# Kernel tuning notes

Measured on AMD Instinct MI355X. Metric: run time of the kernel, lower is better.

The kernel has to match this reference:

```python
import jax, jax.numpy as jnp
import numpy as np

# Ragged layout: 8 sequences packed into total_tokens=6144 tokens.
_SEQLENS = [1024, 512, 1024, 256, 768, 1024, 512, 1024]
_TOTAL = sum(_SEQLENS)  # 6144
_H, _D = 16, 128
_MAXLEN = 1024


def setup_inputs() -> dict:
    key = jax.random.key(0)
    kq, kk, kv = jax.random.split(key, 3)
    cu = jnp.asarray(np.concatenate([[0], np.cumsum(_SEQLENS)]), dtype=jnp.int32)
    return {
        "q": jax.random.normal(kq, (_TOTAL, _H, _D), dtype=jnp.float32),
        "k": jax.random.normal(kk, (_TOTAL, _H, _D), dtype=jnp.float32),
        "v": jax.random.normal(kv, (_TOTAL, _H, _D), dtype=jnp.float32),
        "cu_seqlens_q": cu,
        "cu_seqlens_k": cu,
        "max_seqlen_q": _MAXLEN,
        "max_seqlen_k": _MAXLEN,
    }


def _pad_gather(x, cu, L):
    """Gather packed [T,h,d] into padded [B,L,h,d] plus validity mask [B,L]."""
    starts = cu[:-1]                                   # [B]
    lens = cu[1:] - cu[:-1]                            # [B]
    pos = jnp.arange(L, dtype=cu.dtype)                # [L]
    idx = starts[:, None] + pos[None, :]               # [B,L]
    mask = pos[None, :] < lens[:, None]                # [B,L]
    idx = jnp.clip(idx, 0, x.shape[0] - 1)
    return x[idx], mask, jnp.where(mask, idx, x.shape[0])


def reference(q, k, v, cu_seqlens_q, cu_seqlens_k, max_seqlen_q, max_seqlen_k):
    # Equivalent to pytorch_varlen_attention: per-sequence SDPA (non-causal,
    # no dropout), vectorized via pad-to-max + key masking.
    T, h, d = q.shape
    qp, mq, idx_q = _pad_gather(q, cu_seqlens_q, max_seqlen_q)  # [B,Lq,h,d]
    kp, mk, _ = _pad_gather(k, cu_seqlens_k, max_seqlen_k)      # [B,Lk,h,d]
    vp, _, _ = _pad_gather(v, cu_seqlens_k, max_seqlen_k)

    scale = 1.0 / jnp.sqrt(jnp.asarray(d, dtype=q.dtype))
    scores = jnp.einsum("bqhd,bkhd->bhqk", qp, kp) * scale      # [B,h,Lq,Lk]
    neg = jnp.asarray(jnp.finfo(scores.dtype).min, scores.dtype)
    scores = jnp.where(mk[:, None, None, :], scores, neg)
    attn = jax.nn.softmax(scores, axis=-1)
    out_pad = jnp.einsum("bhqk,bkhd->bqhd", attn, vp)           # [B,Lq,h,d]

    # Scatter valid rows back to packed layout; invalid rows dropped (idx==T).
    out = jnp.zeros((T, h, d), dtype=q.dtype)
    out = out.at[idx_q.reshape(-1)].set(
        out_pad.reshape(-1, h, d), mode="drop")
    return out
```

## Files before the change

### kernel.cpp

```cpp
#include <hip/hip_runtime.h>
#include <hip/hip_bf16.h>
#include <stdint.h>

#define H 16
#define D 128
#define BM 256
#define BN 64
#define NW 8
#define NT 512

typedef __bf16 bf16_t;
typedef bf16_t bf16x8 __attribute__((ext_vector_type(8)));
typedef bf16_t bf16x2 __attribute__((ext_vector_type(2)));
typedef float f32x16 __attribute__((ext_vector_type(16)));

#define MFMA32(a, b, c) __builtin_amdgcn_mfma_f32_32x32x16_bf16(a, b, c, 0, 0, 0)

union FragU { uint32_t w[4]; bf16x8 v; };

static __device__ __forceinline__ uint32_t cvtpk_bf16(float lo, float hi) {
  uint32_t r;
  asm("v_cvt_pk_bf16_f32 %0, %1, %2" : "=v"(r) : "v"(lo), "v"(hi));
  return r;
}

static __device__ __forceinline__ void gld_lds16(const bf16_t* g, bf16_t* l) {
  __builtin_amdgcn_global_load_lds(
      (const __attribute__((address_space(1))) void*)g,
      (__attribute__((address_space(3))) void*)l, 16, 0, 0);
}


__global__ void conv_k(const float* __restrict__ kin, bf16_t* __restrict__ kb, int n8) {
  int i = blockIdx.x * blockDim.x + threadIdx.x;
  int stride = gridDim.x * blockDim.x;
  for (; i < n8; i += stride) {
    const float* p = kin + (size_t)i * 8;
    float4 a = *(const float4*)p, b = *(const float4*)(p + 4);
    bf16x8 w;
    w[0] = (bf16_t)a.x; w[1] = (bf16_t)a.y; w[2] = (bf16_t)a.z; w[3] = (bf16_t)a.w;
    w[4] = (bf16_t)b.x; w[5] = (bf16_t)b.y; w[6] = (bf16_t)b.z; w[7] = (bf16_t)b.w;
    *(bf16x8*)(kb + (size_t)i * 8) = w;
  }
}

__global__ void conv_vt(const float* __restrict__ v, bf16_t* __restrict__ vt,
                        const int* __restrict__ cuk, int nseq) {
  int tile = blockIdx.x, h = blockIdx.y;
  int acc = 0, seq = -1, lt = 0, s0k = 0, Lk = 0, Lkp = 0;
  size_t vb = 0;
  for (int s = 0; s < nseq; ++s) {
    int Ls = cuk[s + 1] - cuk[s];
    int Lp = (Ls + 63) & ~63;
    int nt = Lp / 64;
    if (tile < acc + nt) { seq = s; lt = tile - acc; s0k = cuk[s]; Lk = Ls; Lkp = Lp; break; }
    acc += nt; vb += (size_t)H * D * Lp;
  }
  if (seq < 0) return;
  int kv0 = lt * 64;
  int d = threadIdx.x;
  bf16x8 w[8];
  #pragma unroll
  for (int j = 0; j < 64; ++j) {
    int kv = kv0 + j;
    int kvc = kv < Lk ? kv : Lk - 1;
    float val = v[((size_t)(s0k + kvc) * H + h) * D + d];
    w[j >> 3][j & 7] = (bf16_t)val;
  }
  bf16_t* dstT = vt + vb + (size_t)h * D * Lkp + (size_t)lt * 8192;
  #pragma unroll
  for (int c = 0; c < 8; ++c)
    *(bf16x8*)(dstT + ((size_t)c * 128 + d) * 8) = w[c];
}


__global__ __launch_bounds__(NT, 2)
void fa_varlen11(const float* __restrict__ q,
                 const bf16_t* __restrict__ kb,
                 const bf16_t* __restrict__ vt,
                 const int* __restrict__ cuq,
                 const int* __restrict__ cuk,
                 float* __restrict__ out,
                 int nseq, int maxtiles)
{
  __shared__ alignas(16) bf16_t sK[3][BN * D];
  __shared__ alignas(16) bf16_t sVt[2][8 * 128 * 8];

  const int nwg = gridDim.x;
  const int orig = blockIdx.x;
  const int qq = nwg >> 3, rr = nwg & 7;
  const int xcd = orig & 7;
  const int wgid = (xcd < rr ? xcd * (qq + 1) : rr * (qq + 1) + (xcd - rr) * qq) + (orig >> 3);
  const int tile = wgid % maxtiles;
  const int h = wgid / maxtiles;

  int acc = 0, seq = -1, lt = 0, s0q = 0, s0k = 0, Lq = 0, Lk = 0, Lkp = 0;
  size_t vb = 0;
  for (int s = 0; s < nseq; ++s) {
    int a = cuq[s], b = cuq[s + 1];
    int Ls = b - a;
    int nt = (Ls + BM - 1) / BM;
    int Lks = cuk[s + 1] - cuk[s];
    int Lp = (Lks + 63) & ~63;
    if (tile < acc + nt) {
      seq = s; lt = tile - acc; s0q = a; Lq = Ls;
      s0k = cuk[s]; Lk = Lks; Lkp = Lp;
      break;
    }
    acc += nt; vb += (size_t)H * D * Lp;
  }
  if (seq < 0) return;

  const int q0 = lt * BM;
  const int tid = threadIdx.x;
  const int lane = tid & 63;
  const int lq = lane & 31;
  const int hi = lane >> 5;

  const float SC = 0.08838834764831845f * 1.44269504088896340f;

  bf16x8 qf[8];
  {
    int warp = tid >> 6;
    int qrow = q0 + warp * 32 + lq; if (qrow >= Lq) qrow = Lq - 1;
    const float* qp = q + ((size_t)(s0q + qrow) * H + h) * D;
    #pragma unroll
    for (int ks = 0; ks < 8; ++ks) {
      const float* p = qp + ks * 16 + hi * 8;
      float4 a = *(const float4*)p, b = *(const float4*)(p + 4);
      bf16x8 r;
      r[0] = (bf16_t)(a.x * SC); r[1] = (bf16_t)(a.y * SC);
      r[2] = (bf16_t)(a.z * SC); r[3] = (bf16_t)(a.w * SC);
      r[4] = (bf16_t)(b.x * SC); r[5] = (bf16_t)(b.y * SC);
      r[6] = (bf16_t)(b.z * SC); r[7] = (bf16_t)(b.w * SC);
      qf[ks] = r;
    }
  }

  const bf16_t* vsrcH = vt + vb + (size_t)h * D * Lkp;

  auto STAGE_K = [&](int tt, int buf) {
    const int kvb = tt * BN;
    #pragma unroll
    for (int i = 0; i < 2; ++i) {
      int g = tid + i * NT;
      int row = g >> 4, cc = g & 15;
      int kvr = kvb + row; if (kvr >= Lk) kvr = Lk - 1;
      const bf16_t* src = kb + ((size_t)(s0k + kvr) * H + h) * D + ((cc ^ (row & 7)) << 3);
      gld_lds16(src, &sK[buf][g * 8]);
    }
  };
  auto STAGE_V = [&](int tt, int buf) {
    const bf16_t* vsrc = vsrcH + (size_t)tt * 8192;
    #pragma unroll
    for (int i = 0; i < 2; ++i) {
      int g = tid + i * NT;
      gld_lds16(vsrc + (size_t)g * 8, &sVt[buf][g * 8]);
    }
  };

  f32x16 oacc[4];
  #pragma unroll
  for (int dt = 0; dt < 4; ++dt)
    #pragma unroll
    for (int r = 0; r < 16; ++r) oacc[dt][r] = 0.f;
  float m = -1e30f, l = 0.f;

  const int nkv = (Lk + BN - 1) / BN;

  STAGE_K(0, 0);
  STAGE_V(0, 0);
  STAGE_K(nkv > 1 ? 1 : 0, 1);
  asm volatile("s_waitcnt vmcnt(2)" ::: "memory");
  __builtin_amdgcn_s_barrier();
  __builtin_amdgcn_sched_barrier(0);

  for (int t = 0; t < nkv; ++t) {
    const int kvb = t * BN;
    int tV = t + 1 < nkv ? t + 1 : nkv - 1;
    int tK = t + 2 < nkv ? t + 2 : nkv - 1;
    STAGE_V(tV, (t + 1) & 1);
    STAGE_K(tK, (t + 2) % 3);

    const bf16_t* sKc = sK[t % 3];
    const bf16_t* sVc = sVt[t & 1];
    const bool tail = (kvb + BN > Lk);

    #pragma unroll
    for (int ct = 0; ct < 2; ++ct) {
      f32x16 sa, sb;
      #pragma unroll
      for (int r = 0; r < 16; ++r) { sa[r] = 0.f; sb[r] = 0.f; }
      int krow = ct * 32 + lq;
      __builtin_amdgcn_s_setprio(1);
      #pragma unroll
      for (int ks = 0; ks < 4; ++ks) {
        int posa = (ks * 2 + hi) ^ (krow & 7);
        bf16x8 kfa = *(const bf16x8*)&sKc[krow * 128 + (posa << 3)];
        sa = MFMA32(kfa, qf[ks], sa);
        int posb = ((ks + 4) * 2 + hi) ^ (krow & 7);
        bf16x8 kfb = *(const bf16x8*)&sKc[krow * 128 + (posb << 3)];
        sb = MFMA32(kfb, qf[ks + 4], sb);
      }
      __builtin_amdgcn_s_setprio(0);

      f32x16 st;
      #pragma unroll
      for (int r = 0; r < 16; ++r) {
        float x = sa[r] + sb[r];
        if (tail) {
          int kvi = kvb + ct * 32 + (r & 3) + 8 * (r >> 2) + 4 * hi;
          if (kvi >= Lk) x = -1e30f;
        }
        st[r] = x;
      }
      float m0;
      {
        float a0 = fmaxf(st[0], st[1]),  a1 = fmaxf(st[2], st[3]);
        float a2 = fmaxf(st[4], st[5]),  a3 = fmaxf(st[6], st[7]);
        float a4 = fmaxf(st[8], st[9]),  a5 = fmaxf(st[10], st[11]);
        float a6 = fmaxf(st[12], st[13]), a7 = fmaxf(st[14], st[15]);
        float b0 = fmaxf(a0, a1), b1 = fmaxf(a2, a3);
        float b2 = fmaxf(a4, a5), b3 = fmaxf(a6, a7);
        m0 = fmaxf(fmaxf(b0, b1), fmaxf(b2, b3));
      }
      float m1 = fmaxf(m0, __shfl_xor(m0, 32));
      bool trig = m1 > m + 8.0f;
      float mnew = trig ? m1 : m;
      float alpha = __builtin_amdgcn_exp2f(m - mnew);
      m = mnew;

      #pragma unroll
      for (int r = 0; r < 16; ++r)
        st[r] = __builtin_amdgcn_exp2f(st[r] - m);
      float psum;
      {
        float a0 = st[0] + st[1],  a1 = st[2] + st[3];
        float a2 = st[4] + st[5],  a3 = st[6] + st[7];
        float a4 = st[8] + st[9],  a5 = st[10] + st[11];
        float a6 = st[12] + st[13], a7 = st[14] + st[15];
        float b0 = a0 + a1, b1 = a2 + a3, b2 = a4 + a5, b3 = a6 + a7;
        psum = (b0 + b1) + (b2 + b3);
      }
      psum += __shfl_xor(psum, 32);
      l = l * alpha + psum;

      if (__any(alpha != 1.0f)) {
        #pragma unroll
        for (int r = 0; r < 16; ++r) {
          int cr = (r & 3) + 8 * (r >> 2) + 4 * hi;
          float a2 = __shfl(alpha, cr);
          #pragma unroll
          for (int dt = 0; dt < 4; ++dt) oacc[dt][r] *= a2;
        }
      }

      uint32_t c0 = cvtpk_bf16(st[0],  st[1]),  c1 = cvtpk_bf16(st[2],  st[3]);
      uint32_t c2 = cvtpk_bf16(st[4],  st[5]),  c3 = cvtpk_bf16(st[6],  st[7]);
      uint32_t c4 = cvtpk_bf16(st[8],  st[9]),  c5 = cvtpk_bf16(st[10], st[11]);
      uint32_t c6 = cvtpk_bf16(st[12], st[13]), c7 = cvtpk_bf16(st[14], st[15]);
      { auto rr2 = __builtin_amdgcn_permlane32_swap(c0, c2, false, false); c0 = rr2[0]; c2 = rr2[1]; }
      { auto rr2 = __builtin_amdgcn_permlane32_swap(c1, c3, false, false); c1 = rr2[0]; c3 = rr2[1]; }
      { auto rr2 = __builtin_amdgcn_permlane32_swap(c4, c6, false, false); c4 = rr2[0]; c6 = rr2[1]; }
      { auto rr2 = __builtin_amdgcn_permlane32_swap(c5, c7, false, false); c5 = rr2[0]; c7 = rr2[1]; }
      FragU pa, pb;
      pa.w[0] = c0; pa.w[1] = c1; pa.w[2] = c2; pa.w[3] = c3;
      pb.w[0] = c4; pb.w[1] = c5; pb.w[2] = c6; pb.w[3] = c7;

      __builtin_amdgcn_s_setprio(1);
      #pragma unroll
      for (int dt = 0; dt < 4; ++dt) {
        int drow = dt * 32 + lq;
        bf16x8 vf0 = *(const bf16x8*)&sVc[((ct * 4 + hi) * 128 + drow) << 3];
        oacc[dt] = MFMA32(pa.v, vf0, oacc[dt]);
        bf16x8 vf1 = *(const bf16x8*)&sVc[((ct * 4 + 2 + hi) * 128 + drow) << 3];
        oacc[dt] = MFMA32(pb.v, vf1, oacc[dt]);
      }
      __builtin_amdgcn_s_setprio(0);
    }

    asm volatile("s_waitcnt vmcnt(2)" ::: "memory");
    __builtin_amdgcn_s_barrier();
    __builtin_amdgcn_sched_barrier(0);
  }

  #pragma unroll
  for (int r = 0; r < 16; ++r) {
    int cr = (r & 3) + 8 * (r >> 2) + 4 * hi;
    int warp = tid >> 6;
    int qr = q0 + warp * 32 + cr;
    float lcr = __shfl(l, cr);
    if (qr < Lq) {
      float rn = 1.0f / lcr;
      float* op = out + ((size_t)(s0q + qr) * H + h) * D + lq;
      #pragma unroll
      for (int dt = 0; dt < 4; ++dt)
        op[dt * 32] = oacc[dt][r] * rn;
    }
  }
}


__global__ __launch_bounds__(256, 3)
void fa_varlen2(const float* __restrict__ q,
                const float* __restrict__ k,
                const float* __restrict__ v,
                const int* __restrict__ cuq,
                const int* __restrict__ cuk,
                float* __restrict__ out,
                int nseq)
{
  __shared__ alignas(16) bf16_t sBuf[128 * 128];
  __shared__ float sRed[4 * 32];
  bf16_t* sK  = sBuf;
  bf16_t* sVt = sBuf + 64 * 128;

  const int tile = blockIdx.x;
  const int h = blockIdx.y;

  int acc = 0, seq = -1, lt = 0, s0q = 0, s0k = 0, Lq = 0, Lk = 0;
  for (int s = 0; s < nseq; ++s) {
    int a = cuq[s], b = cuq[s + 1];
    int Ls = b - a;
    int nt = (Ls + 127) / 128;
    if (tile < acc + nt) {
      seq = s; lt = tile - acc; s0q = a; Lq = Ls;
      s0k = cuk[s]; Lk = cuk[s + 1] - s0k;
      break;
    }
    acc += nt;
  }
  if (seq < 0) return;

  const int q0 = lt * 128;
  const int tid = threadIdx.x;
  const int warp = tid >> 6;
  const int lane = tid & 63;
  const int lq = lane & 31;
  const int hi = lane >> 5;

  const float SC = 0.08838834764831845f * 1.44269504088896340f;

  #pragma unroll
  for (int ii = 0; ii < 8; ++ii) {
    int g = tid + ii * 256;
    int row = g >> 4, cc = g & 15;
    int gr = q0 + row; if (gr >= Lq) gr = Lq - 1;
    const float* p = q + ((size_t)(s0q + gr) * H + h) * D + cc * 8;
    float4 f0 = *(const float4*)p;
    float4 f1 = *(const float4*)(p + 4);
    bf16x8 w;
    w[0] = (bf16_t)f0.x; w[1] = (bf16_t)f0.y; w[2] = (bf16_t)f0.z; w[3] = (bf16_t)f0.w;
    w[4] = (bf16_t)f1.x; w[5] = (bf16_t)f1.y; w[6] = (bf16_t)f1.z; w[7] = (bf16_t)f1.w;
    *(bf16x8*)&sBuf[row * 128 + (((cc ^ (row & 7))) << 3)] = w;
  }
  __syncthreads();

  bf16x8 qf[8];
  {
    int row = warp * 32 + lq;
    #pragma unroll
    for (int ks = 0; ks < 8; ++ks) {
      int pos = (ks * 2 + hi) ^ (row & 7);
      qf[ks] = *(const bf16x8*)&sBuf[row * 128 + (pos << 3)];
    }
  }

  f32x16 oacc[4];
  #pragma unroll
  for (int dt = 0; dt < 4; ++dt)
    #pragma unroll
    for (int r = 0; r < 16; ++r) oacc[dt][r] = 0.f;
  float m = -1e30f, l = 0.f;

  const int nkv = (Lk + 63) / 64;
  for (int it = 0; it < nkv; ++it) {
    const int kv0 = it * 64;
    __syncthreads();

    #pragma unroll
    for (int ii = 0; ii < 4; ++ii) {
      int g = tid + ii * 256;
      int row = g >> 4, cc = g & 15;
      int gr = kv0 + row; if (gr >= Lk) gr = Lk - 1;
      const float* p = k + ((size_t)(s0k + gr) * H + h) * D + cc * 8;
      float4 f0 = *(const float4*)p;
      float4 f1 = *(const float4*)(p + 4);
      bf16x8 w;
      w[0] = (bf16_t)f0.x; w[1] = (bf16_t)f0.y; w[2] = (bf16_t)f0.z; w[3] = (bf16_t)f0.w;
      w[4] = (bf16_t)f1.x; w[5] = (bf16_t)f1.y; w[6] = (bf16_t)f1.z; w[7] = (bf16_t)f1.w;
      *(bf16x8*)&sK[row * 128 + (((cc ^ (row & 7))) << 3)] = w;
    }
    {
      int kp = tid & 31;
      int seg = tid >> 5;
      int r0 = kv0 + 2 * kp, r1 = r0 + 1;
      if (r0 >= Lk) r0 = Lk - 1;
      if (r1 >= Lk) r1 = Lk - 1;
      const float* p0 = v + ((size_t)(s0k + r0) * H + h) * D + seg * 16;
      const float* p1 = v + ((size_t)(s0k + r1) * H + h) * D + seg * 16;
      float va[16], vbf[16];
      *(float4*)&va[0]  = *(const float4*)p0;
      *(float4*)&va[4]  = *(const float4*)(p0 + 4);
      *(float4*)&va[8]  = *(const float4*)(p0 + 8);
      *(float4*)&va[12] = *(const float4*)(p0 + 12);
      *(float4*)&vbf[0]  = *(const float4*)p1;
      *(float4*)&vbf[4]  = *(const float4*)(p1 + 4);
      *(float4*)&vbf[8]  = *(const float4*)(p1 + 8);
      *(float4*)&vbf[12] = *(const float4*)(p1 + 12);
      int kvr = 2 * kp;
      #pragma unroll
      for (int i = 0; i < 16; ++i) {
        int d = seg * 16 + i;
        int pos = (kp >> 2) ^ (d & 7);
        bf16x2 w2; w2[0] = (bf16_t)va[i]; w2[1] = (bf16_t)vbf[i];
        *(bf16x2*)&sVt[d * 64 + (pos << 3) + (kvr & 7)] = w2;
      }
    }
    __syncthreads();

    const bool tail = (kv0 + 64 > Lk);

    #pragma unroll
    for (int ct = 0; ct < 2; ++ct) {
      f32x16 st;
      #pragma unroll
      for (int r = 0; r < 16; ++r) st[r] = 0.f;
      int krow = ct * 32 + lq;
      #pragma unroll
      for (int ks = 0; ks < 8; ++ks) {
        int pos = (ks * 2 + hi) ^ (krow & 7);
        bf16x8 kf = *(const bf16x8*)&sK[krow * 128 + (pos << 3)];
        st = MFMA32(kf, qf[ks], st);
      }

      float tmax = -1e30f;
      #pragma unroll
      for (int r = 0; r < 16; ++r) {
        float x = st[r] * SC;
        if (tail) {
          int kvi = kv0 + ct * 32 + (r & 3) + 8 * (r >> 2) + 4 * hi;
          if (kvi >= Lk) x = -1e30f;
        }
        st[r] = x;
        tmax = fmaxf(tmax, x);
      }
      tmax = fmaxf(tmax, __shfl_xor(tmax, 32));
      bool trig = tmax > m + 8.0f;
      float mnew = trig ? tmax : m;
      float alpha = exp2f(m - mnew);
      m = mnew;

      float psum = 0.f;
      #pragma unroll
      for (int r = 0; r < 16; ++r) {
        float e = exp2f(st[r] - m);
        st[r] = e;
        psum += e;
      }
      psum += __shfl_xor(psum, 32);
      l = l * alpha + psum;

      if (__any(alpha != 1.0f)) {
        if (hi == 0) sRed[warp * 32 + lq] = alpha;
        asm volatile("s_waitcnt lgkmcnt(0)" ::: "memory");
        #pragma unroll
        for (int r = 0; r < 16; ++r) {
          float a2 = sRed[warp * 32 + (r & 3) + 8 * (r >> 2) + 4 * hi];
          #pragma unroll
          for (int dt = 0; dt < 4; ++dt) oacc[dt][r] *= a2;
        }
      }

      uint32_t c0 = cvtpk_bf16(st[0],  st[1]),  c1 = cvtpk_bf16(st[2],  st[3]);
      uint32_t c2 = cvtpk_bf16(st[4],  st[5]),  c3 = cvtpk_bf16(st[6],  st[7]);
      uint32_t c4 = cvtpk_bf16(st[8],  st[9]),  c5 = cvtpk_bf16(st[10], st[11]);
      uint32_t c6 = cvtpk_bf16(st[12], st[13]), c7 = cvtpk_bf16(st[14], st[15]);
      { auto rr2 = __builtin_amdgcn_permlane32_swap(c0, c2, false, false); c0 = rr2[0]; c2 = rr2[1]; }
      { auto rr2 = __builtin_amdgcn_permlane32_swap(c1, c3, false, false); c1 = rr2[0]; c3 = rr2[1]; }
      { auto rr2 = __builtin_amdgcn_permlane32_swap(c4, c6, false, false); c4 = rr2[0]; c6 = rr2[1]; }
      { auto rr2 = __builtin_amdgcn_permlane32_swap(c5, c7, false, false); c5 = rr2[0]; c7 = rr2[1]; }
      FragU pa, pb;
      pa.w[0] = c0; pa.w[1] = c1; pa.w[2] = c2; pa.w[3] = c3;
      pb.w[0] = c4; pb.w[1] = c5; pb.w[2] = c6; pb.w[3] = c7;

      #pragma unroll
      for (int dt = 0; dt < 4; ++dt) {
        int drow = dt * 32 + lq;
        int pos0 = (ct * 4 + hi) ^ (drow & 7);
        bf16x8 vf0 = *(const bf16x8*)&sVt[drow * 64 + (pos0 << 3)];
        oacc[dt] = MFMA32(pa.v, vf0, oacc[dt]);
        int pos1 = (ct * 4 + 2 + hi) ^ (drow & 7);
        bf16x8 vf1 = *(const bf16x8*)&sVt[drow * 64 + (pos1 << 3)];
        oacc[dt] = MFMA32(pb.v, vf1, oacc[dt]);
      }
    }
  }

  if (hi == 0) sRed[warp * 32 + lq] = l;
  asm volatile("s_waitcnt lgkmcnt(0)" ::: "memory");
  #pragma unroll
  for (int r = 0; r < 16; ++r) {
    int cr = (r & 3) + 8 * (r >> 2) + 4 * hi;
    int qr = q0 + warp * 32 + cr;
    if (qr < Lq) {
      float rn = 1.0f / sRed[warp * 32 + cr];
      float* op = out + ((size_t)(s0q + qr) * H + h) * D + lq;
      #pragma unroll
      for (int dt = 0; dt < 4; ++dt)
        op[dt * 32] = oacc[dt][r] * rn;
    }
  }
}

extern "C" void kernel_launch(void* const* d_in, const int* in_sizes, int n_in,
                              void* d_out, int out_size, void* d_ws, size_t ws_size,
                              hipStream_t stream) {
  const float* q = (const float*)d_in[0];
  const float* k = (const float*)d_in[1];
  const float* v = (const float*)d_in[2];
  const int* cuq = (const int*)d_in[3];
  const int* cuk = (const int*)d_in[4];
  float* out = (float*)d_out;

  int total = in_sizes[0] / (H * D);
  int nseq = in_sizes[3] - 1;
  int maxtiles = (total + BM - 1) / BM + nseq;

  size_t needK = (size_t)in_sizes[1] * 2;
  size_t needV = (size_t)in_sizes[2] * 2 + (size_t)nseq * 64 * H * D * 2 + 256;

  if (ws_size >= needK + needV) {
    bf16_t* kb = (bf16_t*)d_ws;
    bf16_t* vtb = (bf16_t*)((char*)d_ws + needK);

    conv_k<<<1024, 256, 0, stream>>>(k, kb, in_sizes[1] / 8);
    int maxvt = (total + 63) / 64 + nseq;
    dim3 gvt(maxvt, H);
    conv_vt<<<gvt, 128, 0, stream>>>(v, vtb, cuk, nseq);
    fa_varlen11<<<dim3(maxtiles * H), NT, 0, stream>>>(q, kb, vtb, cuq, cuk, out, nseq, maxtiles);
  } else {
    int mt2 = (total + 127) / 128 + nseq;
    dim3 grid(mt2, H);
    fa_varlen2<<<grid, 256, 0, stream>>>(q, k, v, cuq, cuk, out, nseq);
  }
}
```

Measured before the change: 128.8 us.

## Software-pipeline PV MFMA one sub-tile behind QK and rebalance K/V LDS buffers

The P·V matmul for each 32-key sub-tile is deferred and issued after the next sub-tile's QK^T MFMAs, so the softmax exp/reduce work can overlap matrix-core execution. The rescale by alpha moves along with it. To keep the previous V tile resident, V is now triple-buffered and K double-buffered, and prefetch runs one tile ahead for both instead of two tiles ahead for K. This costs extra registers for the carried P fragments and shortens K prefetch distance, and a drain step after the loop handles the last sub-tile.

```diff
diff --git a/kernel.cpp b/kernel.cpp
--- a/kernel.cpp
+++ b/kernel.cpp
@@ -75,7 +75,7 @@
 
 
 __global__ __launch_bounds__(NT, 2)
-void fa_varlen11(const float* __restrict__ q,
+void fa_varlen12(const float* __restrict__ q,
                  const bf16_t* __restrict__ kb,
                  const bf16_t* __restrict__ vt,
                  const int* __restrict__ cuq,
@@ -83,8 +83,8 @@
                  float* __restrict__ out,
                  int nseq, int maxtiles)
 {
-  __shared__ alignas(16) bf16_t sK[3][BN * D];
-  __shared__ alignas(16) bf16_t sVt[2][8 * 128 * 8];
+  __shared__ alignas(16) bf16_t sK[2][BN * D];
+  __shared__ alignas(16) bf16_t sVt[3][8 * 128 * 8];
 
   const int nwg = gridDim.x;
   const int orig = blockIdx.x;
@@ -166,24 +166,27 @@
     for (int r = 0; r < 16; ++r) oacc[dt][r] = 0.f;
   float m = -1e30f, l = 0.f;
 
+  FragU paP, pbP;
+  #pragma unroll
+  for (int i = 0; i < 4; ++i) { paP.w[i] = 0u; pbP.w[i] = 0u; }
+  float alphaP = 1.0f;
+  int tP = 0, ctP = 0;
+
   const int nkv = (Lk + BN - 1) / BN;
 
   STAGE_K(0, 0);
   STAGE_V(0, 0);
-  STAGE_K(nkv > 1 ? 1 : 0, 1);
-  asm volatile("s_waitcnt vmcnt(2)" ::: "memory");
+  asm volatile("s_waitcnt vmcnt(0)" ::: "memory");
   __builtin_amdgcn_s_barrier();
   __builtin_amdgcn_sched_barrier(0);
 
   for (int t = 0; t < nkv; ++t) {
     const int kvb = t * BN;
-    int tV = t + 1 < nkv ? t + 1 : nkv - 1;
-    int tK = t + 2 < nkv ? t + 2 : nkv - 1;
-    STAGE_V(tV, (t + 1) & 1);
-    STAGE_K(tK, (t + 2) % 3);
-
-    const bf16_t* sKc = sK[t % 3];
-    const bf16_t* sVc = sVt[t & 1];
+    int tn = t + 1 < nkv ? t + 1 : nkv - 1;
+    STAGE_K(tn, (t + 1) & 1);
+    STAGE_V(tn, (t + 1) % 3);
+
+    const bf16_t* sKc = sK[t & 1];
     const bool tail = (kvb + BN > Lk);
 
     #pragma unroll
@@ -203,6 +206,27 @@
         sb = MFMA32(kfb, qf[ks + 4], sb);
       }
       __builtin_amdgcn_s_setprio(0);
+
+      if (__any(alphaP != 1.0f)) {
+        #pragma unroll
+        for (int r = 0; r < 16; ++r) {
+          int cr = (r & 3) + 8 * (r >> 2) + 4 * hi;
+          float a2 = __shfl(alphaP, cr);
+          #pragma unroll
+          for (int dt = 0; dt < 4; ++dt) oacc[dt][r] *= a2;
+        }
+      }
+      {
+        const bf16_t* sVp = sVt[tP % 3];
+        #pragma unroll
+        for (int dt = 0; dt < 4; ++dt) {
+          int drow = dt * 32 + lq;
+          bf16x8 vf0 = *(const bf16x8*)&sVp[((ctP * 4 + hi) * 128 + drow) << 3];
+          oacc[dt] = MFMA32(paP.v, vf0, oacc[dt]);
+          bf16x8 vf1 = *(const bf16x8*)&sVp[((ctP * 4 + 2 + hi) * 128 + drow) << 3];
+          oacc[dt] = MFMA32(pbP.v, vf1, oacc[dt]);
+        }
+      }
 
       f32x16 st;
       #pragma unroll
@@ -245,16 +269,6 @@
       psum += __shfl_xor(psum, 32);
       l = l * alpha + psum;
 
-      if (__any(alpha != 1.0f)) {
-        #pragma unroll
-        for (int r = 0; r < 16; ++r) {
-          int cr = (r & 3) + 8 * (r >> 2) + 4 * hi;
-          float a2 = __shfl(alpha, cr);
-          #pragma unroll
-          for (int dt = 0; dt < 4; ++dt) oacc[dt][r] *= a2;
-        }
-      }
-
       uint32_t c0 = cvtpk_bf16(st[0],  st[1]),  c1 = cvtpk_bf16(st[2],  st[3]);
       uint32_t c2 = cvtpk_bf16(st[4],  st[5]),  c3 = cvtpk_bf16(st[6],  st[7]);
       uint32_t c4 = cvtpk_bf16(st[8],  st[9]),  c5 = cvtpk_bf16(st[10], st[11]);
@@ -263,25 +277,35 @@
       { auto rr2 = __builtin_amdgcn_permlane32_swap(c1, c3, false, false); c1 = rr2[0]; c3 = rr2[1]; }
       { auto rr2 = __builtin_amdgcn_permlane32_swap(c4, c6, false, false); c4 = rr2[0]; c6 = rr2[1]; }
       { auto rr2 = __builtin_amdgcn_permlane32_swap(c5, c7, false, false); c5 = rr2[0]; c7 = rr2[1]; }
-      FragU pa, pb;
-      pa.w[0] = c0; pa.w[1] = c1; pa.w[2] = c2; pa.w[3] = c3;
-      pb.w[0] = c4; pb.w[1] = c5; pb.w[2] = c6; pb.w[3] = c7;
-
-      __builtin_amdgcn_s_setprio(1);
-      #pragma unroll
-      for (int dt = 0; dt < 4; ++dt) {
-        int drow = dt * 32 + lq;
-        bf16x8 vf0 = *(const bf16x8*)&sVc[((ct * 4 + hi) * 128 + drow) << 3];
-        oacc[dt] = MFMA32(pa.v, vf0, oacc[dt]);
-        bf16x8 vf1 = *(const bf16x8*)&sVc[((ct * 4 + 2 + hi) * 128 + drow) << 3];
-        oacc[dt] = MFMA32(pb.v, vf1, oacc[dt]);
-      }
-      __builtin_amdgcn_s_setprio(0);
+      paP.w[0] = c0; paP.w[1] = c1; paP.w[2] = c2; paP.w[3] = c3;
+      pbP.w[0] = c4; pbP.w[1] = c5; pbP.w[2] = c6; pbP.w[3] = c7;
+      alphaP = alpha; tP = t; ctP = ct;
     }
 
     asm volatile("s_waitcnt vmcnt(2)" ::: "memory");
     __builtin_amdgcn_s_barrier();
     __builtin_amdgcn_sched_barrier(0);
+  }
+
+  if (__any(alphaP != 1.0f)) {
+    #pragma unroll
+    for (int r = 0; r < 16; ++r) {
+      int cr = (r & 3) + 8 * (r >> 2) + 4 * hi;
+      float a2 = __shfl(alphaP, cr);
+      #pragma unroll
+      for (int dt = 0; dt < 4; ++dt) oacc[dt][r] *= a2;
+    }
+  }
+  {
+    const bf16_t* sVp = sVt[tP % 3];
+    #pragma unroll
+    for (int dt = 0; dt < 4; ++dt) {
+      int drow = dt * 32 + lq;
+      bf16x8 vf0 = *(const bf16x8*)&sVp[((ctP * 4 + hi) * 128 + drow) << 3];
+      oacc[dt] = MFMA32(paP.v, vf0, oacc[dt]);
+      bf16x8 vf1 = *(const bf16x8*)&sVp[((ctP * 4 + 2 + hi) * 128 + drow) << 3];
+      oacc[dt] = MFMA32(pbP.v, vf1, oacc[dt]);
+    }
   }
 
   #pragma unroll
@@ -538,7 +562,7 @@
     int maxvt = (total + 63) / 64 + nseq;
     dim3 gvt(maxvt, H);
     conv_vt<<<gvt, 128, 0, stream>>>(v, vtb, cuk, nseq);
-    fa_varlen11<<<dim3(maxtiles * H), NT, 0, stream>>>(q, kb, vtb, cuq, cuk, out, nseq, maxtiles);
+    fa_varlen12<<<dim3(maxtiles * H), NT, 0, stream>>>(q, kb, vtb, cuq, cuk, out, nseq, maxtiles);
   } else {
     int mt2 = (total + 127) / 128 + nseq;
     dim3 grid(mt2, H);
```

New measurement: 122.9 us. 4.6% less time.

## Drop LDS staging; read pre-swizzled K and V fragments directly from global

Applied to the files above, without the earlier changes.

K is now pre-converted into a per-tile fragment-major bf16 layout (like V), so each lane's MFMA operand is one contiguous 16-byte global load. The attention kernel then removes all LDS buffers, async global-to-LDS staging and per-iteration barriers, and reads K/V operands straight from global/L2. The Q tile shrinks to 128 rows with 256 threads and 3 blocks per CU, giving more workgroups and no barrier coupling between waves. The risk is that every wave re-reads the same K/V tiles from cache instead of sharing them through LDS, which raises L2 traffic and exposes load latency without explicit prefetch.

```diff
diff --git a/kernel.cpp b/kernel.cpp
--- a/kernel.cpp
+++ b/kernel.cpp
@@ -4,10 +4,9 @@
 
 #define H 16
 #define D 128
-#define BM 256
+#define BM 128
 #define BN 64
-#define NW 8
-#define NT 512
+#define NT 256
 
 typedef __bf16 bf16_t;
 typedef bf16_t bf16x8 __attribute__((ext_vector_type(8)));
@@ -24,23 +23,36 @@
   return r;
 }
 
-static __device__ __forceinline__ void gld_lds16(const bf16_t* g, bf16_t* l) {
-  __builtin_amdgcn_global_load_lds(
-      (const __attribute__((address_space(1))) void*)g,
-      (__attribute__((address_space(3))) void*)l, 16, 0, 0);
-}
-
-
-__global__ void conv_k(const float* __restrict__ kin, bf16_t* __restrict__ kb, int n8) {
-  int i = blockIdx.x * blockDim.x + threadIdx.x;
-  int stride = gridDim.x * blockDim.x;
-  for (; i < n8; i += stride) {
-    const float* p = kin + (size_t)i * 8;
-    float4 a = *(const float4*)p, b = *(const float4*)(p + 4);
-    bf16x8 w;
-    w[0] = (bf16_t)a.x; w[1] = (bf16_t)a.y; w[2] = (bf16_t)a.z; w[3] = (bf16_t)a.w;
-    w[4] = (bf16_t)b.x; w[5] = (bf16_t)b.y; w[6] = (bf16_t)b.z; w[7] = (bf16_t)b.w;
-    *(bf16x8*)(kb + (size_t)i * 8) = w;
+
+__global__ void conv_kc(const float* __restrict__ k, bf16_t* __restrict__ kc,
+                        const int* __restrict__ cuk, int nseq) {
+  int tile = blockIdx.x, h = blockIdx.y;
+  int acc = 0, seq = -1, lt = 0, s0k = 0, Lk = 0, Lkp = 0;
+  size_t vb = 0;
+  for (int s = 0; s < nseq; ++s) {
+    int Ls = cuk[s + 1] - cuk[s];
+    int Lp = (Ls + 63) & ~63;
+    int nt = Lp / 64;
+    if (tile < acc + nt) { seq = s; lt = tile - acc; s0k = cuk[s]; Lk = Ls; Lkp = Lp; break; }
+    acc += nt; vb += (size_t)H * D * Lp;
+  }
+  if (seq < 0) return;
+  int r = threadIdx.x >> 2;
+  int quad = threadIdx.x & 3;
+  int kv = lt * 64 + r; if (kv >= Lk) kv = Lk - 1;
+  const float* p = k + ((size_t)(s0k + kv) * H + h) * D + quad * 32;
+  bf16_t vals[32];
+  #pragma unroll
+  for (int i = 0; i < 8; ++i) {
+    float4 f = *(const float4*)(p + i * 4);
+    vals[i*4+0] = (bf16_t)f.x; vals[i*4+1] = (bf16_t)f.y;
+    vals[i*4+2] = (bf16_t)f.z; vals[i*4+3] = (bf16_t)f.w;
+  }
+  bf16_t* dstT = kc + vb + (size_t)h * D * Lkp + (size_t)lt * 8192;
+  #pragma unroll
+  for (int i = 0; i < 4; ++i) {
+    int c2 = quad * 4 + i;
+    *(bf16x8*)(dstT + ((size_t)c2 * 64 + r) * 8) = *(bf16x8*)&vals[i * 8];
   }
 }
 
@@ -74,18 +86,15 @@
 }
 
 
-__global__ __launch_bounds__(NT, 2)
-void fa_varlen11(const float* __restrict__ q,
-                 const bf16_t* __restrict__ kb,
+__global__ __launch_bounds__(NT, 3)
+void fa_varlen13(const float* __restrict__ q,
+                 const bf16_t* __restrict__ kc,
                  const bf16_t* __restrict__ vt,
                  const int* __restrict__ cuq,
                  const int* __restrict__ cuk,
                  float* __restrict__ out,
                  int nseq, int maxtiles)
 {
-  __shared__ alignas(16) bf16_t sK[3][BN * D];
-  __shared__ alignas(16) bf16_t sVt[2][8 * 128 * 8];
-
   const int nwg = gridDim.x;
   const int orig = blockIdx.x;
   const int qq = nwg >> 3, rr = nwg & 7;
@@ -113,6 +122,7 @@
 
   const int q0 = lt * BM;
   const int tid = threadIdx.x;
+  const int warp = tid >> 6;
   const int lane = tid & 63;
   const int lq = lane & 31;
   const int hi = lane >> 5;
@@ -121,7 +131,6 @@
 
   bf16x8 qf[8];
   {
-    int warp = tid >> 6;
     int qrow = q0 + warp * 32 + lq; if (qrow >= Lq) qrow = Lq - 1;
     const float* qp = q + ((size_t)(s0q + qrow) * H + h) * D;
     #pragma unroll
@@ -137,27 +146,8 @@
     }
   }
 
-  const bf16_t* vsrcH = vt + vb + (size_t)h * D * Lkp;
-
-  auto STAGE_K = [&](int tt, int buf) {
-    const int kvb = tt * BN;
-    #pragma unroll
-    for (int i = 0; i < 2; ++i) {
-      int g = tid + i * NT;
-      int row = g >> 4, cc = g & 15;
-      int kvr = kvb + row; if (kvr >= Lk) kvr = Lk - 1;
-      const bf16_t* src = kb + ((size_t)(s0k + kvr) * H + h) * D + ((cc ^ (row & 7)) << 3);
-      gld_lds16(src, &sK[buf][g * 8]);
-    }
-  };
-  auto STAGE_V = [&](int tt, int buf) {
-    const bf16_t* vsrc = vsrcH + (size_t)tt * 8192;
-    #pragma unroll
-    for (int i = 0; i < 2; ++i) {
-      int g = tid + i * NT;
-      gld_lds16(vsrc + (size_t)g * 8, &sVt[buf][g * 8]);
-    }
-  };
+  const bf16_t* kcH = kc + vb + (size_t)h * D * Lkp;
+  const bf16_t* vtH = vt + vb + (size_t)h * D * Lkp;
 
   f32x16 oacc[4];
   #pragma unroll
@@ -168,22 +158,10 @@
 
   const int nkv = (Lk + BN - 1) / BN;
 
-  STAGE_K(0, 0);
-  STAGE_V(0, 0);
-  STAGE_K(nkv > 1 ? 1 : 0, 1);
-  asm volatile("s_waitcnt vmcnt(2)" ::: "memory");
-  __builtin_amdgcn_s_barrier();
-  __builtin_amdgcn_sched_barrier(0);
-
   for (int t = 0; t < nkv; ++t) {
     const int kvb = t * BN;
-    int tV = t + 1 < nkv ? t + 1 : nkv - 1;
-    int tK = t + 2 < nkv ? t + 2 : nkv - 1;
-    STAGE_V(tV, (t + 1) & 1);
-    STAGE_K(tK, (t + 2) % 3);
-
-    const bf16_t* sKc = sK[t % 3];
-    const bf16_t* sVc = sVt[t & 1];
+    const bf16_t* kcb = kcH + (size_t)t * 8192;
+    const bf16_t* vtb = vtH + (size_t)t * 8192;
     const bool tail = (kvb + BN > Lk);
 
     #pragma unroll
@@ -191,15 +169,12 @@
       f32x16 sa, sb;
       #pragma unroll
       for (int r = 0; r < 16; ++r) { sa[r] = 0.f; sb[r] = 0.f; }
-      int krow = ct * 32 + lq;
       __builtin_amdgcn_s_setprio(1);
       #pragma unroll
       for (int ks = 0; ks < 4; ++ks) {
-        int posa = (ks * 2 + hi) ^ (krow & 7);
-        bf16x8 kfa = *(const bf16x8*)&sKc[krow * 128 + (posa << 3)];
+        bf16x8 kfa = *(const bf16x8*)(kcb + ((((ks * 2 + hi) * 64) + ct * 32 + lq) << 3));
         sa = MFMA32(kfa, qf[ks], sa);
-        int posb = ((ks + 4) * 2 + hi) ^ (krow & 7);
-        bf16x8 kfb = *(const bf16x8*)&sKc[krow * 128 + (posb << 3)];
+        bf16x8 kfb = *(const bf16x8*)(kcb + (((((ks + 4) * 2 + hi) * 64) + ct * 32 + lq) << 3));
         sb = MFMA32(kfb, qf[ks + 4], sb);
       }
       __builtin_amdgcn_s_setprio(0);
@@ -270,24 +245,18 @@
       __builtin_amdgcn_s_setprio(1);
       #pragma unroll
       for (int dt = 0; dt < 4; ++dt) {
-        int drow = dt * 32 + lq;
-        bf16x8 vf0 = *(const bf16x8*)&sVc[((ct * 4 + hi) * 128 + drow) << 3];
+        bf16x8 vf0 = *(const bf16x8*)(vtb + ((((ct * 4 + hi) * 128) + dt * 32 + lq) << 3));
         oacc[dt] = MFMA32(pa.v, vf0, oacc[dt]);
-        bf16x8 vf1 = *(const bf16x8*)&sVc[((ct * 4 + 2 + hi) * 128 + drow) << 3];
+        bf16x8 vf1 = *(const bf16x8*)(vtb + ((((ct * 4 + 2 + hi) * 128) + dt * 32 + lq) << 3));
         oacc[dt] = MFMA32(pb.v, vf1, oacc[dt]);
       }
       __builtin_amdgcn_s_setprio(0);
     }
-
-    asm volatile("s_waitcnt vmcnt(2)" ::: "memory");
-    __builtin_amdgcn_s_barrier();
-    __builtin_amdgcn_sched_barrier(0);
   }
 
   #pragma unroll
   for (int r = 0; r < 16; ++r) {
     int cr = (r & 3) + 8 * (r >> 2) + 4 * hi;
-    int warp = tid >> 6;
     int qr = q0 + warp * 32 + cr;
     float lcr = __shfl(l, cr);
     if (qr < Lq) {
@@ -527,21 +496,21 @@
   int nseq = in_sizes[3] - 1;
   int maxtiles = (total + BM - 1) / BM + nseq;
 
-  size_t needK = (size_t)in_sizes[1] * 2;
-  size_t needV = (size_t)in_sizes[2] * 2 + (size_t)nseq * 64 * H * D * 2 + 256;
+  size_t pad = (size_t)nseq * 64 * H * D * 2 + 256;
+  size_t needK = (size_t)in_sizes[1] * 2 + pad;
+  size_t needV = (size_t)in_sizes[2] * 2 + pad;
 
   if (ws_size >= needK + needV) {
-    bf16_t* kb = (bf16_t*)d_ws;
+    bf16_t* kcb = (bf16_t*)d_ws;
     bf16_t* vtb = (bf16_t*)((char*)d_ws + needK);
 
-    conv_k<<<1024, 256, 0, stream>>>(k, kb, in_sizes[1] / 8);
     int maxvt = (total + 63) / 64 + nseq;
     dim3 gvt(maxvt, H);
+    conv_kc<<<gvt, 256, 0, stream>>>(k, kcb, cuk, nseq);
     conv_vt<<<gvt, 128, 0, stream>>>(v, vtb, cuk, nseq);
-    fa_varlen11<<<dim3(maxtiles * H), NT, 0, stream>>>(q, kb, vtb, cuq, cuk, out, nseq, maxtiles);
+    fa_varlen13<<<dim3(maxtiles * H), NT, 0, stream>>>(q, kcb, vtb, cuq, cuk, out, nseq, maxtiles);
   } else {
-    int mt2 = (total + 127) / 128 + nseq;
-    dim3 grid(mt2, H);
+    dim3 grid(maxtiles, H);
     fa_varlen2<<<grid, 256, 0, stream>>>(q, k, v, cuq, cuk, out, nseq);
   }
 }
```

New measurement: 142.0 us. +10.2%, slower.
